# Performance work log

Hardware: AMD Instinct MI355X
Metric: run time of the kernel (lower is better)

Reference implementation:

```python
import jax, jax.numpy as jnp
import numpy as np

NEG_INF = -1e9
ROUTING_ITERS = 3


def squash(z):
    # z: [B, K, D]
    norm_sq = jnp.sum(z * z, axis=-1, keepdims=True)
    norm = jnp.sqrt(norm_sq + 1e-8)
    return norm_sq / (1.0 + norm_sq) * (z / norm)


def setup_inputs() -> dict:
    key = jax.random.key(0)
    k1, k2, k3, k4 = jax.random.split(key, 4)
    B, L, D, K = 2048, 200, 256, 8
    behavior_embeds = jax.random.normal(k1, (B, L, D), dtype=jnp.float32)
    W = jax.random.normal(k2, (D, D), dtype=jnp.float32) * (1.0 / np.sqrt(D))
    b_init = jax.random.normal(k3, (B, K, L), dtype=jnp.float32)
    mask = jax.random.randint(k4, (B, L), 0, 2, dtype=jnp.int32)
    return {"behavior_embeds": behavior_embeds, "W": W, "b_init": b_init, "mask": mask}


def reference(behavior_embeds, W, b_init, mask):
    # behavior_embeds: [B, L, D]; W: [D, D] (nn.Linear weight, y = x @ W.T)
    u_hat = jnp.einsum('bld,ed->ble', behavior_embeds, W)  # [B, L, D]
    # mask padding positions in routing logits
    b = jnp.where(mask[:, None, :] == 0, NEG_INF, b_init)  # [B, K, L]
    c = None
    for i in range(ROUTING_ITERS):
        w = jax.nn.softmax(b, axis=2)                      # [B, K, L]
        z = jnp.einsum('bkl,bld->bkd', w, u_hat)           # [B, K, D]
        c = squash(z)
        if i < ROUTING_ITERS - 1:
            b = b + jnp.einsum('bkd,bld->bkl', c, u_hat)
    return c
```

## Files before the change

kernel.cpp:

```cpp
#include <hip/hip_runtime.h>
#include <hip/hip_bf16.h>

#define B_ 2048
#define L_ 200
#define D_ 256
#define K_ 8

typedef __attribute__((ext_vector_type(8))) _Float16 half8;
typedef __attribute__((ext_vector_type(4))) _Float16 half4v;
typedef __attribute__((ext_vector_type(4))) float f32x4;

#define LTP 232
#define WP  232
#define CP  264

#define OFF_UTT  0
#define OFF_WH   118784
#define OFF_WL   126208
#define OFF_XA   133632
#define OFF_XB   142080
#define OFF_LB   150528
#define OFF_RED  156928
#define LDS_TOTAL 157472

__global__ __launch_bounds__(256) void w_to_f16(const float* __restrict__ W,
                                                _Float16* __restrict__ Wh) {
    const int idx = (blockIdx.x * 256 + threadIdx.x) * 4;
    const float4 v = *(const float4*)(W + idx);
    half4v h = { (_Float16)v.x, (_Float16)v.y, (_Float16)v.z, (_Float16)v.w };
    *(half4v*)(Wh + idx) = h;
}

__global__ __launch_bounds__(1024, 4) void fused_mie4(
        const float* __restrict__ X, const float* __restrict__ b_init,
        const int* __restrict__ mask, const _Float16* __restrict__ Wh,
        float* __restrict__ out) {
    extern __shared__ char dyn[];
    _Float16* utT = (_Float16*)(dyn + OFF_UTT);
    _Float16* wHs = (_Float16*)(dyn + OFF_WH);
    _Float16* wLs = (_Float16*)(dyn + OFF_WL);
    _Float16* XsA = (_Float16*)(dyn + OFF_XA);
    _Float16* XsB = (_Float16*)(dyn + OFF_XB);
    _Float16* cHs = (_Float16*)(dyn + OFF_XA);
    _Float16* cLs = (_Float16*)(dyn + OFF_XB);
    float* lb   = (float*)(dyn + OFF_LB);
    float* red2 = (float*)(dyn + OFF_RED);

    const int b = blockIdx.x;
    const int t = threadIdx.x;
    const int w = t >> 6, lane = t & 63;
    const int fr = lane & 15, hi = lane >> 4;

    {
        const int row = t >> 2, part = t & 3;
        *(int4*)&utT[row * LTP + 200 + 8 * part] = make_int4(0, 0, 0, 0);
    }
    if (t < 928) *(int4*)(dyn + OFF_WH + 16 * t) = make_int4(0, 0, 0, 0);
    for (int idx = t; idx < K_ * L_; idx += 1024) {
        const int k = idx / L_, l = idx - k * L_;
        lb[idx] = (mask[b * L_ + l] == 0) ? -1e9f
                                          : b_init[(size_t)b * (K_ * L_) + idx];
    }

    half8 bw[8];
    {
        const _Float16* wr = Wh + (size_t)(16 * w + fr) * 256;
#pragma unroll
        for (int d0 = 0; d0 < 8; ++d0)
            bw[d0] = *(const half8*)(wr + 32 * d0 + 8 * hi);
    }

    const float* Xb = X + (size_t)b * L_ * D_;
    const int sc4 = lane * 4;
    {
        const float4 v = *(const float4*)(Xb + w * 256 + sc4);
        half4v h = { (_Float16)v.x, (_Float16)v.y, (_Float16)v.z, (_Float16)v.w };
        *(half4v*)&XsA[w * CP + sc4] = h;
    }
    __syncthreads();

    for (int lt = 0; lt < 13; ++lt) {
        _Float16* cur = (lt & 1) ? XsB : XsA;
        _Float16* nxt = (lt & 1) ? XsA : XsB;
        float4 xv = make_float4(0.f, 0.f, 0.f, 0.f);
        if (lt < 12) {
            const int l = 16 * (lt + 1) + w;
            if (l < L_) xv = *(const float4*)(Xb + l * 256 + sc4);
        }
        f32x4 acc = {};
#pragma unroll
        for (int d0 = 0; d0 < 8; ++d0) {
            const half8 a8 = *(const half8*)&cur[fr * CP + 32 * d0 + 8 * hi];
            acc = __builtin_amdgcn_mfma_f32_16x16x32_f16(bw[d0], a8, acc, 0, 0, 0);
        }
#pragma unroll
        for (int j = 0; j < 4; ++j)
            utT[(16 * w + 4 * hi + j) * LTP + 16 * lt + fr] = (_Float16)acc[j];
        if (lt < 12) {
            half4v h = { (_Float16)xv.x, (_Float16)xv.y, (_Float16)xv.z, (_Float16)xv.w };
            *(half4v*)&nxt[w * CP + sc4] = h;
        }
        __syncthreads();
    }

    half8 zf[7];
#pragma unroll
    for (int ks = 0; ks < 7; ++ks)
        zf[ks] = *(const half8*)&utT[(16 * w + fr) * LTP + 32 * ks + 8 * hi];
    half8 au[8];
    if (w < 13) {
#pragma unroll
        for (int d0 = 0; d0 < 8; ++d0) {
            _Float16 tmp[8];
#pragma unroll
            for (int j = 0; j < 8; ++j)
                tmp[j] = utT[(32 * d0 + 8 * hi + j) * LTP + 16 * w + fr];
            au[d0] = *(half8*)tmp;
        }
    }

    for (int iter = 0; iter < 3; ++iter) {
        if (t < 512) {
            const int k = t >> 6, ln = t & 63;
            float v[4];
            float m = -1e30f;
#pragma unroll
            for (int i = 0; i < 4; ++i) {
                const int l = ln + 64 * i;
                v[i] = (l < L_) ? lb[k * L_ + l] : -1e30f;
                m = fmaxf(m, v[i]);
            }
#pragma unroll
            for (int off = 32; off >= 1; off >>= 1)
                m = fmaxf(m, __shfl_xor(m, off));
            float e[4], s = 0.f;
#pragma unroll
            for (int i = 0; i < 4; ++i) {
                const int l = ln + 64 * i;
                e[i] = (l < L_) ? __expf(v[i] - m) : 0.f;
                s += e[i];
            }
#pragma unroll
            for (int off = 32; off >= 1; off >>= 1)
                s += __shfl_xor(s, off);
            const float rinv = 1.0f / s;
#pragma unroll
            for (int i = 0; i < 4; ++i) {
                const int l = ln + 64 * i;
                if (l < L_) {
                    const float wv = e[i] * rinv;
                    const _Float16 h = (_Float16)wv;
                    wHs[k * WP + l] = h;
                    wLs[k * WP + l] = (_Float16)(wv - (float)h);
                }
            }
        }
        __syncthreads();

        f32x4 zH = {}, zL = {};
#pragma unroll
        for (int ks = 0; ks < 7; ++ks) {
            const half8 ah = *(const half8*)&wHs[fr * WP + 32 * ks + 8 * hi];
            const half8 al = *(const half8*)&wLs[fr * WP + 32 * ks + 8 * hi];
            zH = __builtin_amdgcn_mfma_f32_16x16x32_f16(ah, zf[ks], zH, 0, 0, 0);
            zL = __builtin_amdgcn_mfma_f32_16x16x32_f16(al, zf[ks], zL, 0, 0, 0);
        }
        const float z0 = zH[0] + zL[0], z1 = zH[1] + zL[1];
        const float z2 = zH[2] + zL[2], z3 = zH[3] + zL[3];

        float sq0 = z0 * z0, sq1 = z1 * z1, sq2 = z2 * z2, sq3 = z3 * z3;
#pragma unroll
        for (int off = 1; off <= 8; off <<= 1) {
            sq0 += __shfl_xor(sq0, off);
            sq1 += __shfl_xor(sq1, off);
            sq2 += __shfl_xor(sq2, off);
            sq3 += __shfl_xor(sq3, off);
        }
        if (fr == 0 && hi < 2) {
            f32x4 sv = { sq0, sq1, sq2, sq3 };
            *(f32x4*)&red2[w * 8 + 4 * hi] = sv;
        }
        __syncthreads();

        float myscale = 0.f;
        if (lane < 8) {
            float ns = 0.f;
#pragma unroll
            for (int ww = 0; ww < 16; ++ww) ns += red2[ww * 8 + lane];
            myscale = ns / ((1.f + ns) * sqrtf(ns + 1e-8f));
        }
        const float sc0 = __shfl(myscale, 4 * hi + 0);
        const float sc1 = __shfl(myscale, 4 * hi + 1);
        const float sc2 = __shfl(myscale, 4 * hi + 2);
        const float sc3 = __shfl(myscale, 4 * hi + 3);

        if (iter == 2) {
            if (hi < 2) {
                float* op = out + (size_t)b * (K_ * D_) + (4 * hi) * D_ + 16 * w + fr;
                op[0 * D_] = sc0 * z0;
                op[1 * D_] = sc1 * z1;
                op[2 * D_] = sc2 * z2;
                op[3 * D_] = sc3 * z3;
            }
        } else {
            if (hi < 2) {
                const float v0 = sc0 * z0, v1 = sc1 * z1;
                const float v2 = sc2 * z2, v3 = sc3 * z3;
                const _Float16 h0 = (_Float16)v0, h1 = (_Float16)v1;
                const _Float16 h2 = (_Float16)v2, h3 = (_Float16)v3;
                const int cb = 16 * w + fr;
                cHs[(4 * hi + 0) * CP + cb] = h0;
                cHs[(4 * hi + 1) * CP + cb] = h1;
                cHs[(4 * hi + 2) * CP + cb] = h2;
                cHs[(4 * hi + 3) * CP + cb] = h3;
                cLs[(4 * hi + 0) * CP + cb] = (_Float16)(v0 - (float)h0);
                cLs[(4 * hi + 1) * CP + cb] = (_Float16)(v1 - (float)h1);
                cLs[(4 * hi + 2) * CP + cb] = (_Float16)(v2 - (float)h2);
                cLs[(4 * hi + 3) * CP + cb] = (_Float16)(v3 - (float)h3);
            }
            __syncthreads();

            if (w < 13) {
                f32x4 dH = {}, dL = {};
#pragma unroll
                for (int d0 = 0; d0 < 8; ++d0) {
                    const half8 bh = *(const half8*)&cHs[fr * CP + 32 * d0 + 8 * hi];
                    const half8 bl = *(const half8*)&cLs[fr * CP + 32 * d0 + 8 * hi];
                    dH = __builtin_amdgcn_mfma_f32_16x16x32_f16(au[d0], bh, dH, 0, 0, 0);
                    dL = __builtin_amdgcn_mfma_f32_16x16x32_f16(au[d0], bl, dL, 0, 0, 0);
                }
                if (fr < 8) {
#pragma unroll
                    for (int j = 0; j < 4; ++j) {
                        const int l = 16 * w + 4 * hi + j;
                        if (l < L_) lb[fr * L_ + l] += dH[j] + dL[j];
                    }
                }
            }
            __syncthreads();
        }
    }
}

extern "C" void kernel_launch(void* const* d_in, const int* in_sizes, int n_in,
                              void* d_out, int out_size, void* d_ws, size_t ws_size,
                              hipStream_t stream) {
    (void)in_sizes; (void)n_in; (void)out_size; (void)ws_size;
    const float* behavior = (const float*)d_in[0];
    const float* W        = (const float*)d_in[1];
    const float* b_init   = (const float*)d_in[2];
    const int*   mask     = (const int*)d_in[3];
    float* out      = (float*)d_out;
    _Float16* Wh    = (_Float16*)d_ws;

    hipFuncSetAttribute((const void*)fused_mie4,
                        hipFuncAttributeMaxDynamicSharedMemorySize, LDS_TOTAL);

    w_to_f16<<<64, 256, 0, stream>>>(W, Wh);
    fused_mie4<<<B_, 1024, LDS_TOTAL, stream>>>(behavior, b_init, mask, Wh, out);
}
```

Measured before the change: 261.0 us.

## Pack hi/lo f16 split operands into unused MFMA rows to halve MFMA count

The hi and lo f16 halves of the softmax weights and of the capsule vectors are now packed into the otherwise unused rows 8-15 of a single 16-row MFMA operand, instead of running separate hi and lo MFMAs. The two halves are then combined with cross-lane shuffles. The squash scale is applied after the agreement product rather than before it, so the unscaled z can be written to LDS before the norm reduction, which removes one barrier per iteration. This halves MFMA issue and LDS operand reads, at the cost of extra shuffles and changed padding and LDS layout.

```diff
diff --git a/kernel.cpp b/kernel.cpp
--- a/kernel.cpp
+++ b/kernel.cpp
@@ -10,18 +10,17 @@
 typedef __attribute__((ext_vector_type(4))) _Float16 half4v;
 typedef __attribute__((ext_vector_type(4))) float f32x4;
 
-#define LTP 232
-#define WP  232
+#define LTP 234
+#define WPK 234
 #define CP  264
 
 #define OFF_UTT  0
-#define OFF_WH   118784
-#define OFF_WL   126208
-#define OFF_XA   133632
-#define OFF_XB   142080
-#define OFF_LB   150528
-#define OFF_RED  156928
-#define LDS_TOTAL 157472
+#define OFF_WPK  119808
+#define OFF_XA   127296
+#define OFF_XB   135744
+#define OFF_LB   144192
+#define OFF_RED  150592
+#define LDS_TOTAL 151104
 
 __global__ __launch_bounds__(256) void w_to_f16(const float* __restrict__ W,
                                                 _Float16* __restrict__ Wh) {
@@ -31,18 +30,16 @@
     *(half4v*)(Wh + idx) = h;
 }
 
-__global__ __launch_bounds__(1024, 4) void fused_mie4(
+__global__ __launch_bounds__(1024, 4) void fused_mie6(
         const float* __restrict__ X, const float* __restrict__ b_init,
         const int* __restrict__ mask, const _Float16* __restrict__ Wh,
         float* __restrict__ out) {
     extern __shared__ char dyn[];
-    _Float16* utT = (_Float16*)(dyn + OFF_UTT);
-    _Float16* wHs = (_Float16*)(dyn + OFF_WH);
-    _Float16* wLs = (_Float16*)(dyn + OFF_WL);
-    _Float16* XsA = (_Float16*)(dyn + OFF_XA);
-    _Float16* XsB = (_Float16*)(dyn + OFF_XB);
-    _Float16* cHs = (_Float16*)(dyn + OFF_XA);
-    _Float16* cLs = (_Float16*)(dyn + OFF_XB);
+    _Float16* utT  = (_Float16*)(dyn + OFF_UTT);
+    _Float16* wPk  = (_Float16*)(dyn + OFF_WPK);
+    _Float16* XsA  = (_Float16*)(dyn + OFF_XA);
+    _Float16* XsB  = (_Float16*)(dyn + OFF_XB);
+    _Float16* cPk  = (_Float16*)(dyn + OFF_XA);
     float* lb   = (float*)(dyn + OFF_LB);
     float* red2 = (float*)(dyn + OFF_RED);
 
@@ -51,11 +48,15 @@
     const int w = t >> 6, lane = t & 63;
     const int fr = lane & 15, hi = lane >> 4;
 
-    {
-        const int row = t >> 2, part = t & 3;
-        *(int4*)&utT[row * LTP + 200 + 8 * part] = make_int4(0, 0, 0, 0);
-    }
-    if (t < 928) *(int4*)(dyn + OFF_WH + 16 * t) = make_int4(0, 0, 0, 0);
+#pragma unroll
+    for (int i = 0; i < 2; ++i) {
+        const int n = t + 1024 * i;
+        if (n < 1280) {
+            const int row = n / 5, q = n - 5 * row;
+            *(int4*)&utT[row * LTP + 200 + 8 * q] = make_int4(0, 0, 0, 0);
+        }
+    }
+    if (t < 468) *(int4*)(dyn + OFF_WPK + 16 * t) = make_int4(0, 0, 0, 0);
     for (int idx = t; idx < K_ * L_; idx += 1024) {
         const int k = idx / L_, l = idx - k * L_;
         lb[idx] = (mask[b * L_ + l] == 0) ? -1e9f
@@ -150,24 +151,37 @@
                 if (l < L_) {
                     const float wv = e[i] * rinv;
                     const _Float16 h = (_Float16)wv;
-                    wHs[k * WP + l] = h;
-                    wLs[k * WP + l] = (_Float16)(wv - (float)h);
+                    wPk[k * WPK + l]       = h;
+                    wPk[(k + 8) * WPK + l] = (_Float16)(wv - (float)h);
                 }
             }
         }
         __syncthreads();
 
-        f32x4 zH = {}, zL = {};
+        f32x4 zac = {};
 #pragma unroll
         for (int ks = 0; ks < 7; ++ks) {
-            const half8 ah = *(const half8*)&wHs[fr * WP + 32 * ks + 8 * hi];
-            const half8 al = *(const half8*)&wLs[fr * WP + 32 * ks + 8 * hi];
-            zH = __builtin_amdgcn_mfma_f32_16x16x32_f16(ah, zf[ks], zH, 0, 0, 0);
-            zL = __builtin_amdgcn_mfma_f32_16x16x32_f16(al, zf[ks], zL, 0, 0, 0);
-        }
-        const float z0 = zH[0] + zL[0], z1 = zH[1] + zL[1];
-        const float z2 = zH[2] + zL[2], z3 = zH[3] + zL[3];
-
+            const half8 ap = *(const half8*)&wPk[fr * WPK + 32 * ks + 8 * hi];
+            zac = __builtin_amdgcn_mfma_f32_16x16x32_f16(ap, zf[ks], zac, 0, 0, 0);
+        }
+        const float z0 = zac[0] + __shfl_xor(zac[0], 32);
+        const float z1 = zac[1] + __shfl_xor(zac[1], 32);
+        const float z2 = zac[2] + __shfl_xor(zac[2], 32);
+        const float z3 = zac[3] + __shfl_xor(zac[3], 32);
+
+        if (iter < 2 && hi < 2) {
+            const _Float16 h0 = (_Float16)z0, h1 = (_Float16)z1;
+            const _Float16 h2 = (_Float16)z2, h3 = (_Float16)z3;
+            const int cb = 16 * w + fr;
+            cPk[(4 * hi + 0) * CP + cb] = h0;
+            cPk[(4 * hi + 1) * CP + cb] = h1;
+            cPk[(4 * hi + 2) * CP + cb] = h2;
+            cPk[(4 * hi + 3) * CP + cb] = h3;
+            cPk[(4 * hi + 8)  * CP + cb] = (_Float16)(z0 - (float)h0);
+            cPk[(4 * hi + 9)  * CP + cb] = (_Float16)(z1 - (float)h1);
+            cPk[(4 * hi + 10) * CP + cb] = (_Float16)(z2 - (float)h2);
+            cPk[(4 * hi + 11) * CP + cb] = (_Float16)(z3 - (float)h3);
+        }
         float sq0 = z0 * z0, sq1 = z1 * z1, sq2 = z2 * z2, sq3 = z3 * z3;
 #pragma unroll
         for (int off = 1; off <= 8; off <<= 1) {
@@ -189,12 +203,12 @@
             for (int ww = 0; ww < 16; ++ww) ns += red2[ww * 8 + lane];
             myscale = ns / ((1.f + ns) * sqrtf(ns + 1e-8f));
         }
-        const float sc0 = __shfl(myscale, 4 * hi + 0);
-        const float sc1 = __shfl(myscale, 4 * hi + 1);
-        const float sc2 = __shfl(myscale, 4 * hi + 2);
-        const float sc3 = __shfl(myscale, 4 * hi + 3);
 
         if (iter == 2) {
+            const float sc0 = __shfl(myscale, 4 * hi + 0);
+            const float sc1 = __shfl(myscale, 4 * hi + 1);
+            const float sc2 = __shfl(myscale, 4 * hi + 2);
+            const float sc3 = __shfl(myscale, 4 * hi + 3);
             if (hi < 2) {
                 float* op = out + (size_t)b * (K_ * D_) + (4 * hi) * D_ + 16 * w + fr;
                 op[0 * D_] = sc0 * z0;
@@ -203,38 +217,24 @@
                 op[3 * D_] = sc3 * z3;
             }
         } else {
-            if (hi < 2) {
-                const float v0 = sc0 * z0, v1 = sc1 * z1;
-                const float v2 = sc2 * z2, v3 = sc3 * z3;
-                const _Float16 h0 = (_Float16)v0, h1 = (_Float16)v1;
-                const _Float16 h2 = (_Float16)v2, h3 = (_Float16)v3;
-                const int cb = 16 * w + fr;
-                cHs[(4 * hi + 0) * CP + cb] = h0;
-                cHs[(4 * hi + 1) * CP + cb] = h1;
-                cHs[(4 * hi + 2) * CP + cb] = h2;
-                cHs[(4 * hi + 3) * CP + cb] = h3;
-                cLs[(4 * hi + 0) * CP + cb] = (_Float16)(v0 - (float)h0);
-                cLs[(4 * hi + 1) * CP + cb] = (_Float16)(v1 - (float)h1);
-                cLs[(4 * hi + 2) * CP + cb] = (_Float16)(v2 - (float)h2);
-                cLs[(4 * hi + 3) * CP + cb] = (_Float16)(v3 - (float)h3);
-            }
-            __syncthreads();
-
             if (w < 13) {
-                f32x4 dH = {}, dL = {};
+                f32x4 dac = {};
 #pragma unroll
                 for (int d0 = 0; d0 < 8; ++d0) {
-                    const half8 bh = *(const half8*)&cHs[fr * CP + 32 * d0 + 8 * hi];
-                    const half8 bl = *(const half8*)&cLs[fr * CP + 32 * d0 + 8 * hi];
-                    dH = __builtin_amdgcn_mfma_f32_16x16x32_f16(au[d0], bh, dH, 0, 0, 0);
-                    dL = __builtin_amdgcn_mfma_f32_16x16x32_f16(au[d0], bl, dL, 0, 0, 0);
+                    const half8 bp = *(const half8*)&cPk[fr * CP + 32 * d0 + 8 * hi];
+                    dac = __builtin_amdgcn_mfma_f32_16x16x32_f16(au[d0], bp, dac, 0, 0, 0);
                 }
+                const float d0s = dac[0] + __shfl_xor(dac[0], 8);
+                const float d1s = dac[1] + __shfl_xor(dac[1], 8);
+                const float d2s = dac[2] + __shfl_xor(dac[2], 8);
+                const float d3s = dac[3] + __shfl_xor(dac[3], 8);
+                const float scf = __shfl(myscale, fr & 7);
                 if (fr < 8) {
-#pragma unroll
-                    for (int j = 0; j < 4; ++j) {
-                        const int l = 16 * w + 4 * hi + j;
-                        if (l < L_) lb[fr * L_ + l] += dH[j] + dL[j];
-                    }
+                    const int l0 = 16 * w + 4 * hi;
+                    if (l0 + 0 < L_) lb[fr * L_ + l0 + 0] += d0s * scf;
+                    if (l0 + 1 < L_) lb[fr * L_ + l0 + 1] += d1s * scf;
+                    if (l0 + 2 < L_) lb[fr * L_ + l0 + 2] += d2s * scf;
+                    if (l0 + 3 < L_) lb[fr * L_ + l0 + 3] += d3s * scf;
                 }
             }
             __syncthreads();
@@ -253,9 +253,9 @@
     float* out      = (float*)d_out;
     _Float16* Wh    = (_Float16*)d_ws;
 
-    hipFuncSetAttribute((const void*)fused_mie4,
+    hipFuncSetAttribute((const void*)fused_mie6,
                         hipFuncAttributeMaxDynamicSharedMemorySize, LDS_TOTAL);
 
     w_to_f16<<<64, 256, 0, stream>>>(W, Wh);
-    fused_mie4<<<B_, 1024, LDS_TOTAL, stream>>>(behavior, b_init, mask, Wh, out);
+    fused_mie6<<<B_, 1024, LDS_TOTAL, stream>>>(behavior, b_init, mask, Wh, out);
 }
```

Result: slower. 326.9 us (+25.3%).
